# Performance work log

Measured on AMD Instinct MI355X. Metric: run time of the kernel, lower is better.

The kernel has to match this reference:

```python
import jax, jax.numpy as jnp
import numpy as np

V, E, H, L = 32000, 512, 1024, 2
B, T_DEC, S_ENC = 32, 64, 128
NEG = -1000000.0


def setup_inputs() -> dict:
    key = jax.random.key(0)
    ks = jax.random.split(key, 20)
    s = 0.02
    return {
        "X": jax.random.randint(ks[0], (B, T_DEC), 0, V),
        "enc_outputs": jax.random.normal(ks[1], (B, S_ENC, H), jnp.float32),
        "hidden_state": jax.random.normal(ks[2], (L, B, H), jnp.float32),
        "valid_lens": jax.random.randint(ks[3], (B,), 1, S_ENC),
        "emb": jax.random.normal(ks[4], (V, E), jnp.float32) * s,
        "Wq": jax.random.normal(ks[5], (H, H), jnp.float32) * s,
        "Wk": jax.random.normal(ks[6], (H, H), jnp.float32) * s,
        "wv": jax.random.normal(ks[7], (H,), jnp.float32) * s,
        "W_ih0": jax.random.normal(ks[8], (3 * H, H + E), jnp.float32) * s,
        "W_hh0": jax.random.normal(ks[9], (3 * H, H), jnp.float32) * s,
        "b_ih0": jnp.zeros((3 * H,), jnp.float32),
        "b_hh0": jnp.zeros((3 * H,), jnp.float32),
        "W_ih1": jax.random.normal(ks[10], (3 * H, H), jnp.float32) * s,
        "W_hh1": jax.random.normal(ks[11], (3 * H, H), jnp.float32) * s,
        "b_ih1": jnp.zeros((3 * H,), jnp.float32),
        "b_hh1": jnp.zeros((3 * H,), jnp.float32),
        "W_out": jax.random.normal(ks[12], (V, H), jnp.float32) * s,
        "b_out": jnp.zeros((V,), jnp.float32),
    }


def gru_cell(x, h, W_ih, W_hh, b_ih, b_hh):
    # PyTorch GRU cell gate math
    gi = x @ W_ih.T + b_ih
    gh = h @ W_hh.T + b_hh
    i_r, i_z, i_n = jnp.split(gi, 3, axis=-1)
    h_r, h_z, h_n = jnp.split(gh, 3, axis=-1)
    r = jax.nn.sigmoid(i_r + h_r)
    z = jax.nn.sigmoid(i_z + h_z)
    n = jnp.tanh(i_n + r * h_n)
    return (1.0 - z) * n + z * h


def reference(X, enc_outputs, hidden_state, valid_lens, emb, Wq, Wk, wv,
              W_ih0, W_hh0, b_ih0, b_hh0, W_ih1, W_hh1, b_ih1, b_hh1,
              W_out, b_out):
    # Precompute key projections once (same math as per-step recompute)
    keys_proj = enc_outputs @ Wk.T                       # [B,S,H]
    mask = jnp.arange(S_ENC)[None, :] < valid_lens[:, None]  # [B,S]
    xs = emb[X].transpose(1, 0, 2)                       # [T,B,E]

    def step(h, x_t):
        q = h[-1] @ Wq.T                                 # [B,H] query = top-layer hidden
        scores = jnp.einsum('bsh,h->bs', jnp.tanh(q[:, None, :] + keys_proj), wv)
        scores = jnp.where(mask, scores, NEG)
        attn = jax.nn.softmax(scores, axis=-1)           # [B,S]
        ctx = jnp.einsum('bs,bsh->bh', attn, enc_outputs)
        inp = jnp.concatenate([ctx, x_t], axis=-1)       # [B,H+E]
        h0 = gru_cell(inp, h[0], W_ih0, W_hh0, b_ih0, b_hh0)
        h1 = gru_cell(h0, h[1], W_ih1, W_hh1, b_ih1, b_hh1)
        return jnp.stack([h0, h1]), h1

    _, outs = jax.lax.scan(step, hidden_state, xs)       # outs: [T,B,H]
    logits = outs @ W_out.T + b_out                      # [T,B,V]
    return logits.transpose(1, 0, 2)                     # [B,T,V]
```

## Files before the change

kernel.cpp:

```cpp
#include <hip/hip_runtime.h>


#define BB 32
#define TT 64
#define SS 128
#define HH 1024
#define EE 512
#define VV 32000
#define H3 3072
#define NEGV (-1000000.0f)
#define NB 1024

typedef __attribute__((ext_vector_type(8))) unsigned short u16x8;
typedef __attribute__((ext_vector_type(4))) unsigned short u16x4;
typedef __attribute__((ext_vector_type(8))) short s16x8;
typedef __attribute__((ext_vector_type(4))) float f32x4;

__device__ __forceinline__ unsigned short f2bf(float f) {
  unsigned int u = __builtin_bit_cast(unsigned int, f);
  unsigned int r = (u + 0x7FFFu + ((u >> 16) & 1u)) >> 16;
  return (unsigned short)r;
}
__device__ __forceinline__ float bfu(unsigned short u) {
  return __builtin_bit_cast(float, (unsigned int)u << 16);
}
__device__ __forceinline__ float sigm(float x) {
  return 1.f / (1.f + __expf(-x));
}
__device__ __forceinline__ float tanhfast(float x) {
  float ax = fabsf(x);
  float e = __expf(2.f * ax);
  float th = 1.f - 2.f / (e + 1.f);
  return copysignf(th, x);
}

#if defined(__has_builtin)
#if __has_builtin(__builtin_amdgcn_fdot2_f32_bf16)
#define HAVE_DOT2BF 1
#endif
#endif
#ifdef HAVE_DOT2BF
typedef __attribute__((ext_vector_type(2))) __bf16 bf16x2;
__device__ __forceinline__ float dot2bf(unsigned w, unsigned x, float c) {
  return __builtin_amdgcn_fdot2_f32_bf16(__builtin_bit_cast(bf16x2, w),
                                         __builtin_bit_cast(bf16x2, x), c,
                                         false);
}
#else
__device__ __forceinline__ float dot2bf(unsigned w, unsigned x, float c) {
  c = fmaf(bfu((unsigned short)(w & 0xffffu)),
           bfu((unsigned short)(x & 0xffffu)), c);
  c = fmaf(bfu((unsigned short)(w >> 16)), bfu((unsigned short)(x >> 16)), c);
  return c;
}
#endif
__device__ __forceinline__ void dot8(float& acc, uint4 w, uint4 x) {
  acc = dot2bf(w.x, x.x, acc); acc = dot2bf(w.y, x.y, acc);
  acc = dot2bf(w.z, x.z, acc); acc = dot2bf(w.w, x.w, acc);
}

__device__ __forceinline__ float ldu(const float* p) {
  return __hip_atomic_load((float*)p, __ATOMIC_RELAXED, __HIP_MEMORY_SCOPE_AGENT);
}
__device__ __forceinline__ void stu(float* p, float v) {
  __hip_atomic_store(p, v, __ATOMIC_RELAXED, __HIP_MEMORY_SCOPE_AGENT);
}
__device__ __forceinline__ float2 ldu2(const float* p) {
  unsigned long long v = __hip_atomic_load(
      (const unsigned long long*)p, __ATOMIC_RELAXED, __HIP_MEMORY_SCOPE_AGENT);
  return __builtin_bit_cast(float2, v);
}
__device__ __forceinline__ unsigned long long ldu64(const unsigned short* p) {
  return __hip_atomic_load((const unsigned long long*)p, __ATOMIC_RELAXED,
                           __HIP_MEMORY_SCOPE_AGENT);
}
__device__ __forceinline__ void stu16(unsigned short* p, unsigned short v) {
  __hip_atomic_store(p, v, __ATOMIC_RELAXED, __HIP_MEMORY_SCOPE_AGENT);
}

__global__ __launch_bounds__(256) void k_init(const float* __restrict__ hid,
                                              unsigned short* __restrict__ h0A,
                                              unsigned short* __restrict__ h1i,
                                              unsigned* __restrict__ bar) {
  int i = blockIdx.x * 256 + threadIdx.x;
  if (i < BB * HH) h0A[i] = f2bf(hid[i]);
  else if (i < 2 * BB * HH) h1i[i - BB * HH] = f2bf(hid[i]);
  else if (i < 2 * BB * HH + 16896) bar[i - 2 * BB * HH] = 0u;
}

__global__ __launch_bounds__(256) void k_gather(const int* __restrict__ X,
                                                const float* __restrict__ emb,
                                                unsigned short* __restrict__ xs) {
  int idx = blockIdx.x * 256 + threadIdx.x;
  int r = idx >> 7, c4 = (idx & 127) << 2;
  int td = r >> 5, b = r & 31;
  int tok = X[b * TT + td];
  float4 v = *(const float4*)(emb + (size_t)tok * EE + c4);
  ushort4 o;
  o.x = f2bf(v.x); o.y = f2bf(v.y); o.z = f2bf(v.z); o.w = f2bf(v.w);
  *(ushort4*)(xs + (size_t)r * EE + c4) = o;
}

__global__ __launch_bounds__(256) void k_conv(const float* __restrict__ src,
                                              unsigned short* __restrict__ dst,
                                              int cols4, int ld) {
  int r = blockIdx.x;
  for (int c = threadIdx.x; c < cols4; c += 256) {
    float4 v = *(const float4*)(src + (size_t)r * ld + (size_t)c * 4);
    ushort4 o;
    o.x = f2bf(v.x); o.y = f2bf(v.y); o.z = f2bf(v.z); o.w = f2bf(v.w);
    *(ushort4*)(dst + (size_t)r * cols4 * 4 + (size_t)c * 4) = o;
  }
}

__global__ __launch_bounds__(256) void k_gemm_mfma(
    const unsigned short* __restrict__ A, const unsigned short* __restrict__ W,
    const float* __restrict__ bias, float* __restrict__ C,
    int M, int N, int K, int permuteBT, int outBF16) {
  __shared__ unsigned short As[128 * 32];
  __shared__ unsigned short Bs[128 * 32];
  const int m0 = blockIdx.y * 128, n0 = blockIdx.x * 128;
  const int t = threadIdx.x;
  const int lane = t & 63, w = t >> 6;
  const int wr = w >> 1, wc = w & 1;
  const int fr = lane & 15, fq = lane >> 4;
  const int srow = t >> 2;
  const int scol = (t & 3) * 8;
  f32x4 acc[4][4] = {};
  for (int k0 = 0; k0 < K; k0 += 32) {
#pragma unroll
    for (int i = 0; i < 2; ++i) {
      __builtin_amdgcn_global_load_lds(
          (const __attribute__((address_space(1))) void*)(A + (size_t)(m0 + i * 64 + srow) * K + k0 + scol),
          (__attribute__((address_space(3))) void*)((char*)As + i * 4096 + w * 1024),
          16, 0, 0);
      __builtin_amdgcn_global_load_lds(
          (const __attribute__((address_space(1))) void*)(W + (size_t)(n0 + i * 64 + srow) * K + k0 + scol),
          (__attribute__((address_space(3))) void*)((char*)Bs + i * 4096 + w * 1024),
          16, 0, 0);
    }
    __syncthreads();
    s16x8 af[4], bf[4];
#pragma unroll
    for (int mi = 0; mi < 4; ++mi)
      af[mi] = *(const s16x8*)(As + (wr * 64 + mi * 16 + fr) * 32 + fq * 8);
#pragma unroll
    for (int ni = 0; ni < 4; ++ni)
      bf[ni] = *(const s16x8*)(Bs + (wc * 64 + ni * 16 + fr) * 32 + fq * 8);
#pragma unroll
    for (int mi = 0; mi < 4; ++mi)
#pragma unroll
      for (int ni = 0; ni < 4; ++ni)
        acc[mi][ni] = __builtin_amdgcn_mfma_f32_16x16x32_bf16(
            af[mi], bf[ni], acc[mi][ni], 0, 0, 0);
    __syncthreads();
  }
#pragma unroll
  for (int mi = 0; mi < 4; ++mi) {
#pragma unroll
    for (int ni = 0; ni < 4; ++ni) {
      int gc = n0 + wc * 64 + ni * 16 + fr;
      float bv = bias ? bias[gc] : 0.f;
#pragma unroll
      for (int j = 0; j < 4; ++j) {
        int gm = m0 + wr * 64 + mi * 16 + fq * 4 + j;
        size_t ro = permuteBT ? ((size_t)((gm & 31) * TT + (gm >> 5))) * N
                              : (size_t)gm * N;
        float v = acc[mi][ni][j] + bv;
        if (outBF16) ((unsigned short*)C)[ro + gc] = f2bf(v);
        else         C[ro + gc] = v;
      }
    }
  }
}

__device__ __forceinline__ void gru_phase(
    int sl, int t, unsigned* shmxu, unsigned* shmyu,
    const unsigned short* __restrict__ xg, const unsigned short* __restrict__ hg,
    const unsigned short* __restrict__ wi, const unsigned short* __restrict__ wh,
    const unsigned short* __restrict__ gixrow, const float* __restrict__ bih,
    const float* __restrict__ bhh, unsigned short* __restrict__ hdst) {
  {
    unsigned long long vx = ldu64(xg + t * 4);
    unsigned long long vy = ldu64(hg + t * 4);
    shmxu[t * 2] = (unsigned)vx; shmxu[t * 2 + 1] = (unsigned)(vx >> 32);
    shmyu[t * 2] = (unsigned)vy; shmyu[t * 2 + 1] = (unsigned)(vy >> 32);
  }
  __syncthreads();
  const int nl = t >> 3, q8 = t & 7;
  const int n = sl * 32 + nl;
  const unsigned short* wr = wi + (size_t)n * HH + q8 * 8;
  const unsigned short* hr = wh + (size_t)n * HH + q8 * 8;
  float air = 0, aiz = 0, ain = 0, ahr = 0, ahz = 0, ahn = 0;
#pragma unroll 2
  for (int j = 0; j < 16; ++j) {
    const int ku = q8 * 4 + j * 32;
    uint4 xv = *(const uint4*)(shmxu + ku);
    uint4 yv = *(const uint4*)(shmyu + ku);
    const unsigned short* wj = wr + j * 64;
    const unsigned short* hj = hr + j * 64;
    dot8(air, *(const uint4*)(wj),           xv);
    dot8(aiz, *(const uint4*)(wj + 1048576), xv);
    dot8(ain, *(const uint4*)(wj + 2097152), xv);
    dot8(ahr, *(const uint4*)(hj),           yv);
    dot8(ahz, *(const uint4*)(hj + 1048576), yv);
    dot8(ahn, *(const uint4*)(hj + 2097152), yv);
  }
  air += __shfl_xor(air, 1); air += __shfl_xor(air, 2); air += __shfl_xor(air, 4);
  aiz += __shfl_xor(aiz, 1); aiz += __shfl_xor(aiz, 2); aiz += __shfl_xor(aiz, 4);
  ain += __shfl_xor(ain, 1); ain += __shfl_xor(ain, 2); ain += __shfl_xor(ain, 4);
  ahr += __shfl_xor(ahr, 1); ahr += __shfl_xor(ahr, 2); ahr += __shfl_xor(ahr, 4);
  ahz += __shfl_xor(ahz, 1); ahz += __shfl_xor(ahz, 2); ahz += __shfl_xor(ahz, 4);
  ahn += __shfl_xor(ahn, 1); ahn += __shfl_xor(ahn, 2); ahn += __shfl_xor(ahn, 4);
  if (q8 == 0) {
    float gr = air, gz = aiz, gn = ain;
    if (gixrow) {
      gr += bfu(__builtin_nontemporal_load(gixrow + n));
      gz += bfu(__builtin_nontemporal_load(gixrow + HH + n));
      gn += bfu(__builtin_nontemporal_load(gixrow + 2 * HH + n));
    }
    if (bih) { gr += bih[n]; gz += bih[HH + n]; gn += bih[2 * HH + n]; }
    float h_r = ahr + bhh[n], h_z = ahz + bhh[HH + n], h_n = ahn + bhh[2 * HH + n];
    float r = sigm(gr + h_r);
    float z = sigm(gz + h_z);
    float nn = tanhfast(gn + r * h_n);
    unsigned yw = shmyu[n >> 1];
    float hprev = bfu((unsigned short)((n & 1) ? (yw >> 16) : (yw & 0xffffu)));
    float hv = (1.f - z) * nn + z * hprev;
    stu16(hdst + n, f2bf(hv));
  }
}

__global__ __launch_bounds__(256, 4) void k_persist(
    const unsigned short* __restrict__ keysb,
    const unsigned short* __restrict__ encb,
    const unsigned short* __restrict__ gi0xb,
    const unsigned short* __restrict__ wqb,
    const unsigned short* __restrict__ wi0, const unsigned short* __restrict__ wh0,
    const unsigned short* __restrict__ wi1, const unsigned short* __restrict__ wh1,
    const float* __restrict__ wv, const int* __restrict__ vlen,
    const unsigned short* __restrict__ h1i,
    const float* __restrict__ bhh0, const float* __restrict__ bih1,
    const float* __restrict__ bhh1,
    float* __restrict__ partial,
    unsigned short* __restrict__ ctxb,
    unsigned short* __restrict__ h0A, unsigned short* __restrict__ h0B,
    unsigned short* __restrict__ outsb,
    unsigned* __restrict__ bar) {
  __shared__ unsigned shmxu[512];
  __shared__ unsigned shmyu[512];
  __shared__ float qs[32];
  __shared__ float aux[640];
  __shared__ unsigned short keysl[128 * 32];
  __shared__ unsigned short encl[128 * 32];
  const int bid = blockIdx.x, t = threadIdx.x;
  const int b = bid >> 5, sl = bid & 31;
  const int vb = vlen[b];
  unsigned* rel = bar + 16384;
  unsigned ep = 0;

  for (int i = t; i < 1024; i += 256) {
    int s = i >> 3, q = i & 3;
    if (i & 4) {
      *(u16x4*)(encl + s * 32 + q * 8) =
          *(const u16x4*)(encb + (size_t)(b * SS + s) * HH + sl * 32 + q * 8);
      *(u16x4*)(encl + s * 32 + q * 8 + 4) =
          *(const u16x4*)(encb + (size_t)(b * SS + s) * HH + sl * 32 + q * 8 + 4);
    } else {
      *(u16x4*)(keysl + s * 32 + q * 8) =
          *(const u16x4*)(keysb + (size_t)(b * SS + s) * HH + sl * 32 + q * 8);
      *(u16x4*)(keysl + s * 32 + q * 8 + 4) =
          *(const u16x4*)(keysb + (size_t)(b * SS + s) * HH + sl * 32 + q * 8 + 4);
    }
  }
  __syncthreads();

#define GBAR() do { ++ep; __syncthreads();                                     \
    if (t == 0)                                                                \
      __hip_atomic_store(bar + bid * 16, ep, __ATOMIC_RELAXED,                 \
                         __HIP_MEMORY_SCOPE_AGENT);                            \
    if (sl == 0) {                                                             \
      if (t < 32)                                                              \
        while (__hip_atomic_load(bar + (b * 32 + t) * 16, __ATOMIC_RELAXED,    \
                                 __HIP_MEMORY_SCOPE_AGENT) < ep)               \
          __builtin_amdgcn_s_sleep(1);                                         \
      __syncthreads();                                                         \
      if (t == 0)                                                              \
        __hip_atomic_store(rel + b * 16, ep, __ATOMIC_RELAXED,                 \
                           __HIP_MEMORY_SCOPE_AGENT);                          \
    } else if (t == 0) {                                                       \
      while (__hip_atomic_load(rel + b * 16, __ATOMIC_RELAXED,                 \
                               __HIP_MEMORY_SCOPE_AGENT) < ep)                 \
        __builtin_amdgcn_s_sleep(1);                                           \
    }                                                                          \
    __syncthreads(); } while (0)

  for (int td = 0; td < TT; ++td) {
    const unsigned short* h1old =
        td ? outsb + (size_t)(td - 1) * BB * HH : h1i;
    const unsigned short* h0old = (td & 1) ? h0B : h0A;
    unsigned short*       h0new = (td & 1) ? h0A : h0B;

    {
      {
        unsigned long long vx = ldu64(h1old + b * HH + t * 4);
        shmxu[t * 2] = (unsigned)vx; shmxu[t * 2 + 1] = (unsigned)(vx >> 32);
      }
      __syncthreads();
      {
        const int nl = t >> 3, q8 = t & 7;
        const unsigned short* wr = wqb + (size_t)(sl * 32 + nl) * HH + q8 * 8;
        float acc = 0;
#pragma unroll 4
        for (int j = 0; j < 16; ++j) {
          const int ku = q8 * 4 + j * 32;
          uint4 xv = *(const uint4*)(shmxu + ku);
          dot8(acc, *(const uint4*)(wr + j * 64), xv);
        }
        acc += __shfl_xor(acc, 1); acc += __shfl_xor(acc, 2);
        acc += __shfl_xor(acc, 4);
        if (q8 == 0) qs[nl] = acc;
      }
      __syncthreads();
      const int s = t >> 1, hf = t & 1;
      if (s < vb) {
        const unsigned short* kr = keysl + s * 32 + hf * 16;
        const float* wvp = wv + sl * 32 + hf * 16;
        const float* qp = qs + hf * 16;
        float a = 0;
#pragma unroll
        for (int j = 0; j < 4; ++j) {
          u16x4 kv = *(const u16x4*)(kr + j * 4);
          float4 wvv = *(const float4*)(wvp + j * 4);
          a = fmaf(tanhfast(qp[j * 4 + 0] + bfu(kv[0])), wvv.x, a);
          a = fmaf(tanhfast(qp[j * 4 + 1] + bfu(kv[1])), wvv.y, a);
          a = fmaf(tanhfast(qp[j * 4 + 2] + bfu(kv[2])), wvv.z, a);
          a = fmaf(tanhfast(qp[j * 4 + 3] + bfu(kv[3])), wvv.w, a);
        }
        a += __shfl_xor(a, 1);
        if (hf == 0) stu(partial + ((size_t)(b * SS + s)) * 32 + sl, a);
      }
    }
    GBAR();

    {
      if (t < SS) {
        float sc = NEGV;
        if (t < vb) {
          const float* pp = partial + ((size_t)(b * SS + t)) * 32;
          float s2 = 0;
#pragma unroll
          for (int j = 0; j < 16; ++j) {
            float2 v = ldu2(pp + j * 2);
            s2 += v.x + v.y;
          }
          sc = s2;
        }
        aux[t] = sc;
      }
      __syncthreads();
      float mx = aux[0];
      for (int s = 1; s < vb; ++s) mx = fmaxf(mx, aux[s]);
      float p = (t < SS) ? __expf(aux[t] - mx) : 0.f;
      __syncthreads();
      if (t < SS) aux[t] = p;
      __syncthreads();
      float sum = 0;
      for (int s = 0; s < vb; ++s) sum += aux[s];
      const float inv = 1.f / sum;
      const int cp = t & 15, sg = t >> 4;
      float a0 = 0, a1 = 0;
      const int send = min((sg + 1) * 8, vb);
      for (int s = sg * 8; s < send; ++s) {
        unsigned e2 = *(const unsigned*)(encl + s * 32 + cp * 2);
        float pp = aux[s];
        a0 = fmaf(pp, bfu((unsigned short)(e2 & 0xffffu)), a0);
        a1 = fmaf(pp, bfu((unsigned short)(e2 >> 16)), a1);
      }
      aux[SS + sg * 32 + cp * 2]     = a0;
      aux[SS + sg * 32 + cp * 2 + 1] = a1;
      __syncthreads();
      if (t < 32) {
        float v = 0;
#pragma unroll
        for (int g2 = 0; g2 < 16; ++g2) v += aux[SS + g2 * 32 + t];
        stu16(ctxb + b * HH + sl * 32 + t, f2bf(v * inv));
      }
    }
    GBAR();

    gru_phase(sl, t, shmxu, shmyu, ctxb + b * HH, h0old + b * HH, wi0, wh0,
              gi0xb + ((size_t)td * BB + b) * H3, nullptr, bhh0,
              h0new + b * HH);
    GBAR();

    gru_phase(sl, t, shmxu, shmyu, h0new + b * HH, h1old + b * HH, wi1, wh1,
              nullptr, bih1, bhh1, outsb + (size_t)td * BB * HH + b * HH);
    GBAR();
  }
#undef GBAR
}

extern "C" void kernel_launch(void* const* d_in, const int* in_sizes, int n_in,
                              void* d_out, int out_size, void* d_ws,
                              size_t ws_size, hipStream_t stream) {
  const int*   X    = (const int*)  d_in[0];
  const float* enc  = (const float*)d_in[1];
  const float* hid  = (const float*)d_in[2];
  const int*   vlen = (const int*)  d_in[3];
  const float* emb  = (const float*)d_in[4];
  const float* Wq   = (const float*)d_in[5];
  const float* Wk   = (const float*)d_in[6];
  const float* wv   = (const float*)d_in[7];
  const float* Wih0 = (const float*)d_in[8];
  const float* Whh0 = (const float*)d_in[9];
  const float* bih0 = (const float*)d_in[10];
  const float* bhh0 = (const float*)d_in[11];
  const float* Wih1 = (const float*)d_in[12];
  const float* Whh1 = (const float*)d_in[13];
  const float* bih1 = (const float*)d_in[14];
  const float* bhh1 = (const float*)d_in[15];
  const float* Wout = (const float*)d_in[16];
  const float* bout = (const float*)d_in[17];
  float* out = (float*)d_out;

  float* ws = (float*)d_ws;
  unsigned short* wi0b   = (unsigned short*)ws;
  unsigned short* wh0b   = wi0b + (size_t)3145728;
  unsigned short* wi1b   = wh0b + (size_t)3145728;
  unsigned short* wh1b   = wi1b + (size_t)3145728;
  unsigned short* wqb    = (unsigned short*)(ws + 6291456);
  unsigned short* gi0xb  = (unsigned short*)(ws + 6815744);
  unsigned short* keysb  = (unsigned short*)(ws + 9961472);
  unsigned short* encb   = (unsigned short*)(ws + 12058624);
  unsigned short* xsb    = (unsigned short*)(ws + 14155776);
  unsigned short* wkb    = (unsigned short*)(ws + 14680064);
  unsigned short* wih0xb = (unsigned short*)(ws + 15204352);
  unsigned short* woutb  = (unsigned short*)ws;
  unsigned short* outsb  = (unsigned short*)(ws + 16384000);
  unsigned short* h0A    = (unsigned short*)(ws + 17432576);
  unsigned short* h0B    = (unsigned short*)(ws + 17448960);
  unsigned short* h1i    = (unsigned short*)(ws + 17465344);
  unsigned short* ctxb   = (unsigned short*)(ws + 17481728);
  float*          partial= ws + 17498112;
  unsigned*       bar    = (unsigned*)(ws + 17629184);

  k_init<<<322, 256, 0, stream>>>(hid, h0A, h1i, bar);
  k_gather<<<1024, 256, 0, stream>>>(X, emb, xsb);
  k_conv<<<4096, 256, 0, stream>>>(enc, encb, 256, HH);
  k_conv<<<1024, 256, 0, stream>>>(Wk, wkb, 256, HH);
  k_conv<<<3072, 256, 0, stream>>>(Wih0 + HH, wih0xb, 128, HH + EE);
  k_gemm_mfma<<<dim3(8, 32), 256, 0, stream>>>(encb, wkb, nullptr,
                                               (float*)keysb, BB * SS, HH, HH,
                                               0, 1);
  k_gemm_mfma<<<dim3(24, 16), 256, 0, stream>>>(xsb, wih0xb, bih0,
                                                (float*)gi0xb, TT * BB, H3, EE,
                                                0, 1);
  k_conv<<<1024, 256, 0, stream>>>(Wq, wqb, 256, HH);
  k_conv<<<3072, 256, 0, stream>>>(Wih0, wi0b, 256, HH + EE);
  k_conv<<<3072, 256, 0, stream>>>(Whh0, wh0b, 256, HH);
  k_conv<<<3072, 256, 0, stream>>>(Wih1, wi1b, 256, HH);
  k_conv<<<3072, 256, 0, stream>>>(Whh1, wh1b, 256, HH);

  k_persist<<<NB, 256, 0, stream>>>(keysb, encb, gi0xb, wqb,
                                    wi0b, wh0b, wi1b, wh1b,
                                    wv, vlen, h1i,
                                    bhh0, bih1, bhh1,
                                    partial, ctxb, h0A, h0B, outsb, bar);

  k_conv<<<32000, 256, 0, stream>>>(Wout, woutb, 256, HH);
  k_gemm_mfma<<<dim3(250, 16), 256, 0, stream>>>(outsb, woutb, bout, out,
                                                 TT * BB, VV, HH, 1, 0);
}
```

Baseline: 4.480 ms.

## Replace per-batch GRU dot products with MFMA batched gate GEMMs in persistent kernel

The GRU phases no longer compute each batch row's gate dot products with scalar bf16 dot8 across all blocks. 96 blocks now run an MFMA GEMM over the whole batch, so each weight row is read once per step instead of once per batch element. Gate results go to fp32 scratch buffers, and a separate elementwise phase on 128 blocks applies the gate math. This adds two extra grid barriers per step and replaces the per-batch hierarchical barrier with a single-master one that spins on 1024 flags. The scratch buffers reuse workspace that earlier held xs, wkb and wih0x.

```diff
diff --git a/kernel.cpp b/kernel.cpp
--- a/kernel.cpp
+++ b/kernel.cpp
@@ -15,6 +15,7 @@
 typedef __attribute__((ext_vector_type(4))) unsigned short u16x4;
 typedef __attribute__((ext_vector_type(8))) short s16x8;
 typedef __attribute__((ext_vector_type(4))) float f32x4;
+typedef __attribute__((ext_vector_type(2))) unsigned long long u64x2;
 
 __device__ __forceinline__ unsigned short f2bf(float f) {
   unsigned int u = __builtin_bit_cast(unsigned int, f);
@@ -74,6 +75,10 @@
   return __hip_atomic_load((const unsigned long long*)p, __ATOMIC_RELAXED,
                            __HIP_MEMORY_SCOPE_AGENT);
 }
+__device__ __forceinline__ unsigned short ldu16(const unsigned short* p) {
+  return __hip_atomic_load((unsigned short*)p, __ATOMIC_RELAXED,
+                           __HIP_MEMORY_SCOPE_AGENT);
+}
 __device__ __forceinline__ void stu16(unsigned short* p, unsigned short v) {
   __hip_atomic_store(p, v, __ATOMIC_RELAXED, __HIP_MEMORY_SCOPE_AGENT);
 }
@@ -85,7 +90,7 @@
   int i = blockIdx.x * 256 + threadIdx.x;
   if (i < BB * HH) h0A[i] = f2bf(hid[i]);
   else if (i < 2 * BB * HH) h1i[i - BB * HH] = f2bf(hid[i]);
-  else if (i < 2 * BB * HH + 16896) bar[i - 2 * BB * HH] = 0u;
+  else if (i < 2 * BB * HH + 17472) bar[i - 2 * BB * HH] = 0u;
 }
 
 __global__ __launch_bounds__(256) void k_gather(const int* __restrict__ X,
@@ -174,60 +179,35 @@
   }
 }
 
-__device__ __forceinline__ void gru_phase(
-    int sl, int t, unsigned* shmxu, unsigned* shmyu,
-    const unsigned short* __restrict__ xg, const unsigned short* __restrict__ hg,
-    const unsigned short* __restrict__ wi, const unsigned short* __restrict__ wh,
-    const unsigned short* __restrict__ gixrow, const float* __restrict__ bih,
-    const float* __restrict__ bhh, unsigned short* __restrict__ hdst) {
-  {
-    unsigned long long vx = ldu64(xg + t * 4);
-    unsigned long long vy = ldu64(hg + t * 4);
-    shmxu[t * 2] = (unsigned)vx; shmxu[t * 2 + 1] = (unsigned)(vx >> 32);
-    shmyu[t * 2] = (unsigned)vy; shmyu[t * 2 + 1] = (unsigned)(vy >> 32);
-  }
-  __syncthreads();
-  const int nl = t >> 3, q8 = t & 7;
-  const int n = sl * 32 + nl;
-  const unsigned short* wr = wi + (size_t)n * HH + q8 * 8;
-  const unsigned short* hr = wh + (size_t)n * HH + q8 * 8;
-  float air = 0, aiz = 0, ain = 0, ahr = 0, ahz = 0, ahn = 0;
-#pragma unroll 2
-  for (int j = 0; j < 16; ++j) {
-    const int ku = q8 * 4 + j * 32;
-    uint4 xv = *(const uint4*)(shmxu + ku);
-    uint4 yv = *(const uint4*)(shmyu + ku);
-    const unsigned short* wj = wr + j * 64;
-    const unsigned short* hj = hr + j * 64;
-    dot8(air, *(const uint4*)(wj),           xv);
-    dot8(aiz, *(const uint4*)(wj + 1048576), xv);
-    dot8(ain, *(const uint4*)(wj + 2097152), xv);
-    dot8(ahr, *(const uint4*)(hj),           yv);
-    dot8(ahz, *(const uint4*)(hj + 1048576), yv);
-    dot8(ahn, *(const uint4*)(hj + 2097152), yv);
-  }
-  air += __shfl_xor(air, 1); air += __shfl_xor(air, 2); air += __shfl_xor(air, 4);
-  aiz += __shfl_xor(aiz, 1); aiz += __shfl_xor(aiz, 2); aiz += __shfl_xor(aiz, 4);
-  ain += __shfl_xor(ain, 1); ain += __shfl_xor(ain, 2); ain += __shfl_xor(ain, 4);
-  ahr += __shfl_xor(ahr, 1); ahr += __shfl_xor(ahr, 2); ahr += __shfl_xor(ahr, 4);
-  ahz += __shfl_xor(ahz, 1); ahz += __shfl_xor(ahz, 2); ahz += __shfl_xor(ahz, 4);
-  ahn += __shfl_xor(ahn, 1); ahn += __shfl_xor(ahn, 2); ahn += __shfl_xor(ahn, 4);
-  if (q8 == 0) {
-    float gr = air, gz = aiz, gn = ain;
-    if (gixrow) {
-      gr += bfu(__builtin_nontemporal_load(gixrow + n));
-      gz += bfu(__builtin_nontemporal_load(gixrow + HH + n));
-      gn += bfu(__builtin_nontemporal_load(gixrow + 2 * HH + n));
-    }
-    if (bih) { gr += bih[n]; gz += bih[HH + n]; gn += bih[2 * HH + n]; }
-    float h_r = ahr + bhh[n], h_z = ahz + bhh[HH + n], h_n = ahn + bhh[2 * HH + n];
-    float r = sigm(gr + h_r);
-    float z = sigm(gz + h_z);
-    float nn = tanhfast(gn + r * h_n);
-    unsigned yw = shmyu[n >> 1];
-    float hprev = bfu((unsigned short)((n & 1) ? (yw >> 16) : (yw & 0xffffu)));
-    float hv = (1.f - z) * nn + z * hprev;
-    stu16(hdst + n, f2bf(hv));
+__device__ __forceinline__ void gemm_slice(
+    int rbase, int lane,
+    const unsigned short* __restrict__ Wi, const unsigned short* __restrict__ Wh,
+    const unsigned short* __restrict__ Ai, const unsigned short* __restrict__ Ah,
+    float* __restrict__ Di, float* __restrict__ Dh) {
+  const bool ih = rbase < H3;
+  const unsigned short* W = ih ? Wi : Wh;
+  const unsigned short* A = ih ? Ai : Ah;
+  float* D = ih ? Di : Dh;
+  const int rw = ih ? rbase : rbase - H3;
+  const int fr = lane & 15, fq = lane >> 4;
+  const unsigned short* wrow = W + (size_t)(rw + fr) * HH + fq * 8;
+  const unsigned short* ar0 = A + (size_t)fr * HH + fq * 8;
+  const unsigned short* ar1 = A + (size_t)(16 + fr) * HH + fq * 8;
+  f32x4 acc0 = {0.f, 0.f, 0.f, 0.f}, acc1 = {0.f, 0.f, 0.f, 0.f};
+  for (int ks = 0; ks < 32; ++ks) {
+    s16x8 bfr = *(const s16x8*)(wrow + ks * 32);
+    u64x2 a0, a1;
+    a0.x = ldu64(ar0 + ks * 32); a0.y = ldu64(ar0 + ks * 32 + 4);
+    a1.x = ldu64(ar1 + ks * 32); a1.y = ldu64(ar1 + ks * 32 + 4);
+    acc0 = __builtin_amdgcn_mfma_f32_16x16x32_bf16(
+        __builtin_bit_cast(s16x8, a0), bfr, acc0, 0, 0, 0);
+    acc1 = __builtin_amdgcn_mfma_f32_16x16x32_bf16(
+        __builtin_bit_cast(s16x8, a1), bfr, acc1, 0, 0, 0);
+  }
+#pragma unroll
+  for (int j = 0; j < 4; ++j) {
+    stu(D + (size_t)(fq * 4 + j) * H3 + rw + fr, acc0[j]);
+    stu(D + (size_t)(16 + fq * 4 + j) * H3 + rw + fr, acc1[j]);
   }
 }
 
@@ -243,12 +223,13 @@
     const float* __restrict__ bhh0, const float* __restrict__ bih1,
     const float* __restrict__ bhh1,
     float* __restrict__ partial,
+    float* __restrict__ gi0f, float* __restrict__ gh0f,
+    float* __restrict__ gi1f, float* __restrict__ gh1f,
     unsigned short* __restrict__ ctxb,
     unsigned short* __restrict__ h0A, unsigned short* __restrict__ h0B,
     unsigned short* __restrict__ outsb,
     unsigned* __restrict__ bar) {
   __shared__ unsigned shmxu[512];
-  __shared__ unsigned shmyu[512];
   __shared__ float qs[32];
   __shared__ float aux[640];
   __shared__ unsigned short keysl[128 * 32];
@@ -279,17 +260,18 @@
     if (t == 0)                                                                \
       __hip_atomic_store(bar + bid * 16, ep, __ATOMIC_RELAXED,                 \
                          __HIP_MEMORY_SCOPE_AGENT);                            \
-    if (sl == 0) {                                                             \
-      if (t < 32)                                                              \
-        while (__hip_atomic_load(bar + (b * 32 + t) * 16, __ATOMIC_RELAXED,    \
+    if (bid == 0) {                                                            \
+      _Pragma("unroll")                                                        \
+      for (int g = 0; g < 4; ++g)                                              \
+        while (__hip_atomic_load(bar + (t + 256 * g) * 16, __ATOMIC_RELAXED,   \
                                  __HIP_MEMORY_SCOPE_AGENT) < ep)               \
           __builtin_amdgcn_s_sleep(1);                                         \
       __syncthreads();                                                         \
-      if (t == 0)                                                              \
-        __hip_atomic_store(rel + b * 16, ep, __ATOMIC_RELAXED,                 \
+      if (t < 64)                                                              \
+        __hip_atomic_store(rel + t * 16, ep, __ATOMIC_RELAXED,                 \
                            __HIP_MEMORY_SCOPE_AGENT);                          \
     } else if (t == 0) {                                                       \
-      while (__hip_atomic_load(rel + b * 16, __ATOMIC_RELAXED,                 \
+      while (__hip_atomic_load(rel + (bid >> 4) * 16, __ATOMIC_RELAXED,        \
                                __HIP_MEMORY_SCOPE_AGENT) < ep)                 \
         __builtin_amdgcn_s_sleep(1);                                           \
     }                                                                          \
@@ -389,13 +371,52 @@
     }
     GBAR();
 
-    gru_phase(sl, t, shmxu, shmyu, ctxb + b * HH, h0old + b * HH, wi0, wh0,
-              gi0xb + ((size_t)td * BB + b) * H3, nullptr, bhh0,
-              h0new + b * HH);
+    if (bid < 96)
+      gemm_slice(bid * 64 + (t >> 6) * 16, t & 63, wi0, wh0,
+                 ctxb, h0old, gi0f, gh0f);
     GBAR();
 
-    gru_phase(sl, t, shmxu, shmyu, h0new + b * HH, h1old + b * HH, wi1, wh1,
-              nullptr, bih1, bhh1, outsb + (size_t)td * BB * HH + b * HH);
+    if (bid < 128) {
+      const int idx = (bid << 8) + t;
+      const int eb = idx >> 10, n = idx & 1023;
+      const size_t g3 = (size_t)eb * H3 + n;
+      const unsigned short* gx = gi0xb + ((size_t)td * BB + eb) * H3;
+      float gr = ldu(gi0f + g3)        + bfu(__builtin_nontemporal_load(gx + n));
+      float gz = ldu(gi0f + g3 + 1024) + bfu(__builtin_nontemporal_load(gx + HH + n));
+      float gn = ldu(gi0f + g3 + 2048) + bfu(__builtin_nontemporal_load(gx + 2 * HH + n));
+      float hr = ldu(gh0f + g3)        + bhh0[n];
+      float hz = ldu(gh0f + g3 + 1024) + bhh0[HH + n];
+      float hn = ldu(gh0f + g3 + 2048) + bhh0[2 * HH + n];
+      float r = sigm(gr + hr);
+      float z = sigm(gz + hz);
+      float nn = tanhfast(gn + r * hn);
+      float hp = bfu(ldu16(h0old + eb * HH + n));
+      stu16(h0new + eb * HH + n, f2bf((1.f - z) * nn + z * hp));
+    }
+    GBAR();
+
+    if (bid < 96)
+      gemm_slice(bid * 64 + (t >> 6) * 16, t & 63, wi1, wh1,
+                 h0new, h1old, gi1f, gh1f);
+    GBAR();
+
+    if (bid < 128) {
+      const int idx = (bid << 8) + t;
+      const int eb = idx >> 10, n = idx & 1023;
+      const size_t g3 = (size_t)eb * H3 + n;
+      float gr = ldu(gi1f + g3)        + bih1[n];
+      float gz = ldu(gi1f + g3 + 1024) + bih1[HH + n];
+      float gn = ldu(gi1f + g3 + 2048) + bih1[2 * HH + n];
+      float hr = ldu(gh1f + g3)        + bhh1[n];
+      float hz = ldu(gh1f + g3 + 1024) + bhh1[HH + n];
+      float hn = ldu(gh1f + g3 + 2048) + bhh1[2 * HH + n];
+      float r = sigm(gr + hr);
+      float z = sigm(gz + hz);
+      float nn = tanhfast(gn + r * hn);
+      float hp = bfu(ldu16(h1old + eb * HH + n));
+      stu16(outsb + (size_t)td * BB * HH + eb * HH + n,
+            f2bf((1.f - z) * nn + z * hp));
+    }
     GBAR();
   }
 #undef GBAR
@@ -436,6 +457,10 @@
   unsigned short* xsb    = (unsigned short*)(ws + 14155776);
   unsigned short* wkb    = (unsigned short*)(ws + 14680064);
   unsigned short* wih0xb = (unsigned short*)(ws + 15204352);
+  float*          gi0f   = ws + 14155776;
+  float*          gh0f   = gi0f + 98304;
+  float*          gi1f   = gh0f + 98304;
+  float*          gh1f   = gi1f + 98304;
   unsigned short* woutb  = (unsigned short*)ws;
   unsigned short* outsb  = (unsigned short*)(ws + 16384000);
   unsigned short* h0A    = (unsigned short*)(ws + 17432576);
@@ -445,7 +470,7 @@
   float*          partial= ws + 17498112;
   unsigned*       bar    = (unsigned*)(ws + 17629184);
 
-  k_init<<<322, 256, 0, stream>>>(hid, h0A, h1i, bar);
+  k_init<<<325, 256, 0, stream>>>(hid, h0A, h1i, bar);
   k_gather<<<1024, 256, 0, stream>>>(X, emb, xsb);
   k_conv<<<4096, 256, 0, stream>>>(enc, encb, 256, HH);
   k_conv<<<1024, 256, 0, stream>>>(Wk, wkb, 256, HH);
@@ -466,7 +491,8 @@
                                     wi0b, wh0b, wi1b, wh1b,
                                     wv, vlen, h1i,
                                     bhh0, bih1, bhh1,
-                                    partial, ctxb, h0A, h0B, outsb, bar);
+                                    partial, gi0f, gh0f, gi1f, gh1f,
+                                    ctxb, h0A, h0B, outsb, bar);
 
   k_conv<<<32000, 256, 0, stream>>>(Wout, woutb, 256, HH);
   k_gemm_mfma<<<dim3(250, 16), 256, 0, stream>>>(outsb, woutb, bout, out,
```

Result: slower. 5.340 ms (+19.2%).

## Retile GRU phase so each block serves 4 batch rows; use a global grid barrier

Applied to the files above, without the earlier changes.

The GRU phases are re-partitioned. Each block now computes 8 hidden units for 4 batch rows instead of 32 units for one batch row, so every weight row read from global memory is reused across 4 batch elements in shared memory. This cuts redundant weight traffic per step. Because the new mapping spans batches, the per-batch barrier is replaced by a full-grid barrier: block 0 polls all 1024 flags and releases 64 flags. That adds barrier latency and more shared memory for the staged inputs.

```diff
diff --git a/kernel.cpp b/kernel.cpp
--- a/kernel.cpp
+++ b/kernel.cpp
@@ -85,7 +85,7 @@
   int i = blockIdx.x * 256 + threadIdx.x;
   if (i < BB * HH) h0A[i] = f2bf(hid[i]);
   else if (i < 2 * BB * HH) h1i[i - BB * HH] = f2bf(hid[i]);
-  else if (i < 2 * BB * HH + 16896) bar[i - 2 * BB * HH] = 0u;
+  else if (i < 2 * BB * HH + 17472) bar[i - 2 * BB * HH] = 0u;
 }
 
 __global__ __launch_bounds__(256) void k_gather(const int* __restrict__ X,
@@ -175,28 +175,34 @@
 }
 
 __device__ __forceinline__ void gru_phase(
-    int sl, int t, unsigned* shmxu, unsigned* shmyu,
+    int bid, int t, unsigned* sx, unsigned* sy,
     const unsigned short* __restrict__ xg, const unsigned short* __restrict__ hg,
     const unsigned short* __restrict__ wi, const unsigned short* __restrict__ wh,
-    const unsigned short* __restrict__ gixrow, const float* __restrict__ bih,
+    const unsigned short* __restrict__ gixbase, const float* __restrict__ bih,
     const float* __restrict__ bhh, unsigned short* __restrict__ hdst) {
-  {
-    unsigned long long vx = ldu64(xg + t * 4);
-    unsigned long long vy = ldu64(hg + t * 4);
-    shmxu[t * 2] = (unsigned)vx; shmxu[t * 2 + 1] = (unsigned)(vx >> 32);
-    shmyu[t * 2] = (unsigned)vy; shmyu[t * 2 + 1] = (unsigned)(vy >> 32);
+  const int n0 = (bid & 127) * 8;
+  const int bbase = (bid >> 7) * 4;
+  for (int i = t; i < 2048; i += 256) {
+    int r = i >> 8, c = i & 255;
+    int bl = r & 3;
+    const unsigned short* src =
+        ((r < 4) ? xg : hg) + (size_t)(bbase + bl) * HH + c * 4;
+    unsigned long long v = ldu64(src);
+    unsigned* dst = ((r < 4) ? sx : sy) + bl * 512 + c * 2;
+    dst[0] = (unsigned)v; dst[1] = (unsigned)(v >> 32);
   }
   __syncthreads();
-  const int nl = t >> 3, q8 = t & 7;
-  const int n = sl * 32 + nl;
-  const unsigned short* wr = wi + (size_t)n * HH + q8 * 8;
-  const unsigned short* hr = wh + (size_t)n * HH + q8 * 8;
+  const int nl = t >> 5, bl = (t >> 3) & 3, k8 = t & 7;
+  const int n = n0 + nl;
+  const unsigned short* wr = wi + (size_t)n * HH + k8 * 8;
+  const unsigned short* hr = wh + (size_t)n * HH + k8 * 8;
+  const unsigned* xrow = sx + bl * 512 + k8 * 4;
+  const unsigned* yrow = sy + bl * 512 + k8 * 4;
   float air = 0, aiz = 0, ain = 0, ahr = 0, ahz = 0, ahn = 0;
-#pragma unroll 2
+#pragma unroll 4
   for (int j = 0; j < 16; ++j) {
-    const int ku = q8 * 4 + j * 32;
-    uint4 xv = *(const uint4*)(shmxu + ku);
-    uint4 yv = *(const uint4*)(shmyu + ku);
+    uint4 xv = *(const uint4*)(xrow + j * 32);
+    uint4 yv = *(const uint4*)(yrow + j * 32);
     const unsigned short* wj = wr + j * 64;
     const unsigned short* hj = hr + j * 64;
     dot8(air, *(const uint4*)(wj),           xv);
@@ -212,22 +218,23 @@
   ahr += __shfl_xor(ahr, 1); ahr += __shfl_xor(ahr, 2); ahr += __shfl_xor(ahr, 4);
   ahz += __shfl_xor(ahz, 1); ahz += __shfl_xor(ahz, 2); ahz += __shfl_xor(ahz, 4);
   ahn += __shfl_xor(ahn, 1); ahn += __shfl_xor(ahn, 2); ahn += __shfl_xor(ahn, 4);
-  if (q8 == 0) {
+  if (k8 == 0) {
+    const int gb = bbase + bl;
     float gr = air, gz = aiz, gn = ain;
-    if (gixrow) {
-      gr += bfu(__builtin_nontemporal_load(gixrow + n));
-      gz += bfu(__builtin_nontemporal_load(gixrow + HH + n));
-      gn += bfu(__builtin_nontemporal_load(gixrow + 2 * HH + n));
+    if (gixbase) {
+      const unsigned short* gx = gixbase + (size_t)gb * H3;
+      gr += bfu(__builtin_nontemporal_load(gx + n));
+      gz += bfu(__builtin_nontemporal_load(gx + HH + n));
+      gn += bfu(__builtin_nontemporal_load(gx + 2 * HH + n));
     }
     if (bih) { gr += bih[n]; gz += bih[HH + n]; gn += bih[2 * HH + n]; }
     float h_r = ahr + bhh[n], h_z = ahz + bhh[HH + n], h_n = ahn + bhh[2 * HH + n];
     float r = sigm(gr + h_r);
     float z = sigm(gz + h_z);
     float nn = tanhfast(gn + r * h_n);
-    unsigned yw = shmyu[n >> 1];
-    float hprev = bfu((unsigned short)((n & 1) ? (yw >> 16) : (yw & 0xffffu)));
-    float hv = (1.f - z) * nn + z * hprev;
-    stu16(hdst + n, f2bf(hv));
+    unsigned yw = sy[bl * 512 + (n >> 1)];
+    float hp = bfu((unsigned short)((n & 1) ? (yw >> 16) : (yw & 0xffffu)));
+    stu16(hdst + (size_t)gb * HH + n, f2bf((1.f - z) * nn + z * hp));
   }
 }
 
@@ -247,8 +254,8 @@
     unsigned short* __restrict__ h0A, unsigned short* __restrict__ h0B,
     unsigned short* __restrict__ outsb,
     unsigned* __restrict__ bar) {
-  __shared__ unsigned shmxu[512];
-  __shared__ unsigned shmyu[512];
+  __shared__ __align__(16) unsigned sx[2048];
+  __shared__ __align__(16) unsigned sy[2048];
   __shared__ float qs[32];
   __shared__ float aux[640];
   __shared__ unsigned short keysl[128 * 32];
@@ -279,17 +286,18 @@
     if (t == 0)                                                                \
       __hip_atomic_store(bar + bid * 16, ep, __ATOMIC_RELAXED,                 \
                          __HIP_MEMORY_SCOPE_AGENT);                            \
-    if (sl == 0) {                                                             \
-      if (t < 32)                                                              \
-        while (__hip_atomic_load(bar + (b * 32 + t) * 16, __ATOMIC_RELAXED,    \
+    if (bid == 0) {                                                            \
+      _Pragma("unroll")                                                        \
+      for (int g = 0; g < 4; ++g)                                              \
+        while (__hip_atomic_load(bar + (t + 256 * g) * 16, __ATOMIC_RELAXED,   \
                                  __HIP_MEMORY_SCOPE_AGENT) < ep)               \
           __builtin_amdgcn_s_sleep(1);                                         \
       __syncthreads();                                                         \
-      if (t == 0)                                                              \
-        __hip_atomic_store(rel + b * 16, ep, __ATOMIC_RELAXED,                 \
+      if (t < 64)                                                              \
+        __hip_atomic_store(rel + t * 16, ep, __ATOMIC_RELAXED,                 \
                            __HIP_MEMORY_SCOPE_AGENT);                          \
     } else if (t == 0) {                                                       \
-      while (__hip_atomic_load(rel + b * 16, __ATOMIC_RELAXED,                 \
+      while (__hip_atomic_load(rel + (bid >> 4) * 16, __ATOMIC_RELAXED,        \
                                __HIP_MEMORY_SCOPE_AGENT) < ep)                 \
         __builtin_amdgcn_s_sleep(1);                                           \
     }                                                                          \
@@ -304,7 +312,7 @@
     {
       {
         unsigned long long vx = ldu64(h1old + b * HH + t * 4);
-        shmxu[t * 2] = (unsigned)vx; shmxu[t * 2 + 1] = (unsigned)(vx >> 32);
+        sx[t * 2] = (unsigned)vx; sx[t * 2 + 1] = (unsigned)(vx >> 32);
       }
       __syncthreads();
       {
@@ -314,7 +322,7 @@
 #pragma unroll 4
         for (int j = 0; j < 16; ++j) {
           const int ku = q8 * 4 + j * 32;
-          uint4 xv = *(const uint4*)(shmxu + ku);
+          uint4 xv = *(const uint4*)(sx + ku);
           dot8(acc, *(const uint4*)(wr + j * 64), xv);
         }
         acc += __shfl_xor(acc, 1); acc += __shfl_xor(acc, 2);
@@ -389,13 +397,12 @@
     }
     GBAR();
 
-    gru_phase(sl, t, shmxu, shmyu, ctxb + b * HH, h0old + b * HH, wi0, wh0,
-              gi0xb + ((size_t)td * BB + b) * H3, nullptr, bhh0,
-              h0new + b * HH);
+    gru_phase(bid, t, sx, sy, ctxb, h0old, wi0, wh0,
+              gi0xb + (size_t)td * BB * H3, nullptr, bhh0, h0new);
     GBAR();
 
-    gru_phase(sl, t, shmxu, shmyu, h0new + b * HH, h1old + b * HH, wi1, wh1,
-              nullptr, bih1, bhh1, outsb + (size_t)td * BB * HH + b * HH);
+    gru_phase(bid, t, sx, sy, h0new, h1old, wi1, wh1,
+              nullptr, bih1, bhh1, outsb + (size_t)td * BB * HH);
     GBAR();
   }
 #undef GBAR
@@ -445,7 +452,7 @@
   float*          partial= ws + 17498112;
   unsigned*       bar    = (unsigned*)(ws + 17629184);
 
-  k_init<<<322, 256, 0, stream>>>(hid, h0A, h1i, bar);
+  k_init<<<325, 256, 0, stream>>>(hid, h0A, h1i, bar);
   k_gather<<<1024, 256, 0, stream>>>(X, emb, xsb);
   k_conv<<<4096, 256, 0, stream>>>(enc, encb, 256, HH);
   k_conv<<<1024, 256, 0, stream>>>(Wk, wkb, 256, HH);
```

After: 5.099 ms. 1.14x slower.

## Distribute score reduction across blocks and cache previous hidden states in shared memory

Applied to the files above, without the earlier changes.

Each block now reduces the 32 partial attention sums for its own 4 sequence positions using wave shuffles and writes them to a new global scores buffer. The softmax phase then reads the finished scores, so each of the 32 blocks serving a batch row no longer repeats the full 128×32 reduction. This adds an extra grid-wide barrier per timestep. Separately, the previous hidden states h0 and h1 are loaded into dedicated shared buffers once per step and reused by the GRU phases, removing redundant global loads.

```diff
diff --git a/kernel.cpp b/kernel.cpp
--- a/kernel.cpp
+++ b/kernel.cpp
@@ -64,11 +64,6 @@
 }
 __device__ __forceinline__ void stu(float* p, float v) {
   __hip_atomic_store(p, v, __ATOMIC_RELAXED, __HIP_MEMORY_SCOPE_AGENT);
-}
-__device__ __forceinline__ float2 ldu2(const float* p) {
-  unsigned long long v = __hip_atomic_load(
-      (const unsigned long long*)p, __ATOMIC_RELAXED, __HIP_MEMORY_SCOPE_AGENT);
-  return __builtin_bit_cast(float2, v);
 }
 __device__ __forceinline__ unsigned long long ldu64(const unsigned short* p) {
   return __hip_atomic_load((const unsigned long long*)p, __ATOMIC_RELAXED,
@@ -175,16 +170,14 @@
 }
 
 __device__ __forceinline__ void gru_phase(
-    int sl, int t, unsigned* shmxu, unsigned* shmyu,
-    const unsigned short* __restrict__ xg, const unsigned short* __restrict__ hg,
+    int sl, int t, unsigned* sxu, const unsigned* syu,
+    const unsigned short* __restrict__ xg,
     const unsigned short* __restrict__ wi, const unsigned short* __restrict__ wh,
     const unsigned short* __restrict__ gixrow, const float* __restrict__ bih,
     const float* __restrict__ bhh, unsigned short* __restrict__ hdst) {
   {
     unsigned long long vx = ldu64(xg + t * 4);
-    unsigned long long vy = ldu64(hg + t * 4);
-    shmxu[t * 2] = (unsigned)vx; shmxu[t * 2 + 1] = (unsigned)(vx >> 32);
-    shmyu[t * 2] = (unsigned)vy; shmyu[t * 2 + 1] = (unsigned)(vy >> 32);
+    sxu[t * 2] = (unsigned)vx; sxu[t * 2 + 1] = (unsigned)(vx >> 32);
   }
   __syncthreads();
   const int nl = t >> 3, q8 = t & 7;
@@ -195,8 +188,8 @@
 #pragma unroll 2
   for (int j = 0; j < 16; ++j) {
     const int ku = q8 * 4 + j * 32;
-    uint4 xv = *(const uint4*)(shmxu + ku);
-    uint4 yv = *(const uint4*)(shmyu + ku);
+    uint4 xv = *(const uint4*)(sxu + ku);
+    uint4 yv = *(const uint4*)(syu + ku);
     const unsigned short* wj = wr + j * 64;
     const unsigned short* hj = hr + j * 64;
     dot8(air, *(const uint4*)(wj),           xv);
@@ -224,10 +217,9 @@
     float r = sigm(gr + h_r);
     float z = sigm(gz + h_z);
     float nn = tanhfast(gn + r * h_n);
-    unsigned yw = shmyu[n >> 1];
-    float hprev = bfu((unsigned short)((n & 1) ? (yw >> 16) : (yw & 0xffffu)));
-    float hv = (1.f - z) * nn + z * hprev;
-    stu16(hdst + n, f2bf(hv));
+    unsigned yw = syu[n >> 1];
+    float hp = bfu((unsigned short)((n & 1) ? (yw >> 16) : (yw & 0xffffu)));
+    stu16(hdst + n, f2bf((1.f - z) * nn + z * hp));
   }
 }
 
@@ -242,13 +234,14 @@
     const unsigned short* __restrict__ h1i,
     const float* __restrict__ bhh0, const float* __restrict__ bih1,
     const float* __restrict__ bhh1,
-    float* __restrict__ partial,
+    float* __restrict__ partial, float* __restrict__ scores,
     unsigned short* __restrict__ ctxb,
     unsigned short* __restrict__ h0A, unsigned short* __restrict__ h0B,
     unsigned short* __restrict__ outsb,
     unsigned* __restrict__ bar) {
-  __shared__ unsigned shmxu[512];
-  __shared__ unsigned shmyu[512];
+  __shared__ unsigned sh1u[512];
+  __shared__ unsigned sh0u[512];
+  __shared__ unsigned sxu[512];
   __shared__ float qs[32];
   __shared__ float aux[640];
   __shared__ unsigned short keysl[128 * 32];
@@ -303,8 +296,10 @@
 
     {
       {
-        unsigned long long vx = ldu64(h1old + b * HH + t * 4);
-        shmxu[t * 2] = (unsigned)vx; shmxu[t * 2 + 1] = (unsigned)(vx >> 32);
+        unsigned long long v1 = ldu64(h1old + b * HH + t * 4);
+        unsigned long long v0 = ldu64(h0old + b * HH + t * 4);
+        sh1u[t * 2] = (unsigned)v1; sh1u[t * 2 + 1] = (unsigned)(v1 >> 32);
+        sh0u[t * 2] = (unsigned)v0; sh0u[t * 2 + 1] = (unsigned)(v0 >> 32);
       }
       __syncthreads();
       {
@@ -314,7 +309,7 @@
 #pragma unroll 4
         for (int j = 0; j < 16; ++j) {
           const int ku = q8 * 4 + j * 32;
-          uint4 xv = *(const uint4*)(shmxu + ku);
+          uint4 xv = *(const uint4*)(sh1u + ku);
           dot8(acc, *(const uint4*)(wr + j * 64), xv);
         }
         acc += __shfl_xor(acc, 1); acc += __shfl_xor(acc, 2);
@@ -343,21 +338,20 @@
     }
     GBAR();
 
+    if (t < 128) {
+      const int s = sl * 4 + (t >> 5), g = t & 31;
+      float a = 0;
+      if (s < vb) {
+        a = ldu(partial + ((size_t)(b * SS + s)) * 32 + g);
+        a += __shfl_xor(a, 1); a += __shfl_xor(a, 2); a += __shfl_xor(a, 4);
+        a += __shfl_xor(a, 8); a += __shfl_xor(a, 16);
+      }
+      if (g == 0) stu(scores + b * SS + s, (s < vb) ? a : NEGV);
+    }
+    GBAR();
+
     {
-      if (t < SS) {
-        float sc = NEGV;
-        if (t < vb) {
-          const float* pp = partial + ((size_t)(b * SS + t)) * 32;
-          float s2 = 0;
-#pragma unroll
-          for (int j = 0; j < 16; ++j) {
-            float2 v = ldu2(pp + j * 2);
-            s2 += v.x + v.y;
-          }
-          sc = s2;
-        }
-        aux[t] = sc;
-      }
+      if (t < SS) aux[t] = ldu(scores + b * SS + t);
       __syncthreads();
       float mx = aux[0];
       for (int s = 1; s < vb; ++s) mx = fmaxf(mx, aux[s]);
@@ -389,12 +383,12 @@
     }
     GBAR();
 
-    gru_phase(sl, t, shmxu, shmyu, ctxb + b * HH, h0old + b * HH, wi0, wh0,
+    gru_phase(sl, t, sxu, sh0u, ctxb + b * HH, wi0, wh0,
               gi0xb + ((size_t)td * BB + b) * H3, nullptr, bhh0,
               h0new + b * HH);
     GBAR();
 
-    gru_phase(sl, t, shmxu, shmyu, h0new + b * HH, h1old + b * HH, wi1, wh1,
+    gru_phase(sl, t, sxu, sh1u, h0new + b * HH, wi1, wh1,
               nullptr, bih1, bhh1, outsb + (size_t)td * BB * HH + b * HH);
     GBAR();
   }
@@ -443,7 +437,8 @@
   unsigned short* h1i    = (unsigned short*)(ws + 17465344);
   unsigned short* ctxb   = (unsigned short*)(ws + 17481728);
   float*          partial= ws + 17498112;
-  unsigned*       bar    = (unsigned*)(ws + 17629184);
+  float*          scores = ws + 17629184;
+  unsigned*       bar    = (unsigned*)(ws + 17633280);
 
   k_init<<<322, 256, 0, stream>>>(hid, h0A, h1i, bar);
   k_gather<<<1024, 256, 0, stream>>>(X, emb, xsb);
@@ -466,7 +461,7 @@
                                     wi0b, wh0b, wi1b, wh1b,
                                     wv, vlen, h1i,
                                     bhh0, bih1, bhh1,
-                                    partial, ctxb, h0A, h0B, outsb, bar);
+                                    partial, scores, ctxb, h0A, h0B, outsb, bar);
 
   k_conv<<<32000, 256, 0, stream>>>(Wout, woutb, 256, HH);
   k_gemm_mfma<<<dim3(250, 16), 256, 0, stream>>>(outsb, woutb, bout, out,
```

After: 4.420 ms (median of 2 runs). About the same (-1.3%).
